# Performance work log

Measured on AMD Instinct MI355X. Metric: run time of the kernel, lower is better.

The kernel has to match this reference:

```python
import jax, jax.numpy as jnp
import numpy as np
from jax.scipy.linalg import solve_triangular, cho_solve

N, NT, O, L1, L2 = 8192, 512, 9, 3, 3
LOG2PI = float(np.log(2.0 * np.pi))


def setup_inputs() -> dict:
    key = jax.random.key(0)
    ks = jax.random.split(key, 10)
    return {
        "y": jax.random.normal(ks[0], (N, NT, O), jnp.float32),
        "b1_r1": 0.5 * jax.random.normal(ks[1], (L1,), jnp.float32),
        "lambda_r1_free": jax.random.normal(ks[2], (6,), jnp.float32),
        "q_r1_diag": jax.random.uniform(ks[3], (L1,), jnp.float32),
        "b1_r2": 0.3 * jax.random.normal(ks[4], (L2, L2), jnp.float32),
        "lambda_r2_free": jax.random.normal(ks[5], (O - 1,), jnp.float32),
        "q_r2_diag": jax.random.uniform(ks[6], (L2,), jnp.float32),
        "r_diag": jax.random.uniform(ks[7], (O,), jnp.float32),
        "gamma1": jnp.array([4.0], jnp.float32),
        "gamma2": jax.random.normal(ks[8], (L1,), jnp.float32),
        "gamma3": jnp.array([4.0], jnp.float32),
        "gamma4": jax.random.normal(ks[9], (L2,), jnp.float32),
    }


def _rskf_nll(y, b1_r1, lambda_r1_free, q_r1_diag, b1_r2, lambda_r2_free,
              q_r2_diag, r_diag, gamma1, gamma2, gamma3, gamma4):
    Nn, Nt, Oo = y.shape
    dt = y.dtype
    # Regime-1 structural matrices (3-factor CFA measurement model)
    B1 = jnp.diag(b1_r1)
    Lam1 = jnp.zeros((Oo, L1), dt)
    Lam1 = Lam1.at[0, 0].set(1.0).at[3, 1].set(1.0).at[6, 2].set(1.0)
    Lam1 = Lam1.at[1, 0].set(lambda_r1_free[0]).at[2, 0].set(lambda_r1_free[1])
    Lam1 = Lam1.at[4, 1].set(lambda_r1_free[2]).at[5, 1].set(lambda_r1_free[3])
    Lam1 = Lam1.at[7, 2].set(lambda_r1_free[4]).at[8, 2].set(lambda_r1_free[5])
    Q1 = jnp.diag(jnp.abs(q_r1_diag) + 1e-4)
    # Regime-2: full transition matrix, 1-factor loading column
    B2 = b1_r2
    Lam2 = jnp.zeros((Oo, L2), dt).at[0, 0].set(1.0).at[1:, 0].set(lambda_r2_free)
    Q2 = jnp.diag(jnp.abs(q_r2_diag) + 1e-4)
    R = jnp.diag(jnp.abs(r_diag) + 1e-4)
    eyeO = jnp.eye(Oo, dtype=dt)

    def regime_step(eta, P, B, Lam, Q, y_t):
        # eta:(N,L) P:(N,L,L) y_t:(N,O)
        L = B.shape[0]
        eta_p = eta @ B.T
        P_p = jnp.einsum('ij,njk,lk->nil', B, P, B) + Q
        mu = eta_p @ Lam.T
        v = y_t - mu
        F = jnp.einsum('ij,njk,lk->nil', Lam, P_p, Lam) + R    # (N,O,O)
        chol = jnp.linalg.cholesky(F)
        z = solve_triangular(chol, v[..., None], lower=True)[..., 0]
        logdet = 2.0 * jnp.sum(jnp.log(jnp.diagonal(chol, axis1=-2, axis2=-1)), axis=-1)
        loglik = -0.5 * (Oo * LOG2PI + logdet + jnp.sum(z * z, axis=-1))
        # F is SPD (R has positive diagonal), so pinv == inverse via Cholesky
        Finv = cho_solve((chol, True), jnp.broadcast_to(eyeO, F.shape))
        K = P_p @ Lam.T @ Finv                                  # (N,L,O)
        eta_f = eta_p + jnp.einsum('nlo,no->nl', K, v)
        ImKL = jnp.eye(L, dtype=dt) - K @ Lam
        P_f = ImKL @ P_p @ jnp.swapaxes(ImKL, -1, -2) + K @ R @ jnp.swapaxes(K, -1, -2)
        return eta_f, P_f, loglik

    def step(carry, y_t):
        eta1, P1, eta2, P2, m_prob, ll = carry
        p11 = jax.nn.sigmoid(gamma1 + eta1 @ gamma2)            # (N,)
        p22 = jax.nn.sigmoid(gamma3 + eta2 @ gamma4)
        T = jnp.stack([jnp.stack([p11, 1.0 - p11], -1),
                       jnp.stack([1.0 - p22, p22], -1)], axis=1)  # (N,2,2)
        m_pred = jnp.einsum('nij,ni->nj', T, m_prob)
        eta1f, P1f, ll1 = regime_step(eta1, P1, B1, Lam1, Q1, y_t)
        eta2f, P2f, ll2 = regime_step(eta2, P2, B2, Lam2, Q2, y_t)
        log_joint = jnp.stack([ll1, ll2], -1) + jnp.log(m_pred + 1e-9)
        log_marg = jax.scipy.special.logsumexp(log_joint, axis=-1)
        m_new = jnp.exp(log_joint - log_marg[:, None])
        return (eta1f, P1f, eta2f, P2f, m_new, ll + log_marg.sum()), None

    eta1_0 = jnp.zeros((Nn, L1), dt)
    P1_0 = jnp.broadcast_to(jnp.eye(L1, dtype=dt) * 1000.0, (Nn, L1, L1))
    eta2_0 = jnp.zeros((Nn, L2), dt)
    P2_0 = jnp.broadcast_to(jnp.eye(L2, dtype=dt) * 1000.0, (Nn, L2, L2))
    m0 = jnp.broadcast_to(jnp.array([0.99, 0.01], dt), (Nn, 2))  # informative prior
    carry0 = (eta1_0, P1_0, eta2_0, P2_0, m0, jnp.zeros((), dt))
    carry, _ = jax.lax.scan(jax.checkpoint(step), carry0, jnp.transpose(y, (1, 0, 2)))
    return -carry[5]


def reference(y, b1_r1, lambda_r1_free, q_r1_diag, b1_r2, lambda_r2_free,
              q_r2_diag, r_diag, gamma1, gamma2, gamma3, gamma4):
    return _rskf_nll(y, b1_r1, lambda_r1_free, q_r1_diag, b1_r2, lambda_r2_free,
                     q_r2_diag, r_diag, gamma1, gamma2, gamma3, gamma4)
```

## Files before the change

### kernel.cpp

```cpp
#include <hip/hip_runtime.h>
#include <math.h>

#define NSUBJ 8192
#define NTT   512
#define OBS   9
#define LOG2PI 1.8378770664093453f

#define CHUNKS   16
#define REALSTEP 32
#define WARMSTEP 32
#define SERIAL_P 48
#define LDS_ENT  68

__global__ void zero_out_kernel(float* out) { out[0] = 0.0f; }

__device__ __forceinline__ float fast_rcp(float x) { return __builtin_amdgcn_rcpf(x); }

__device__ __forceinline__ float swap1(float x) {
    int r = __builtin_amdgcn_update_dpp(0, __float_as_int(x), 0xB1, 0xF, 0xF, true);
    return __int_as_float(r);
}

__global__ __launch_bounds__(64, 1) void precomp_kernel(
    const float* __restrict__ b1_r1, const float* __restrict__ lam1f,
    const float* __restrict__ q1d,   const float* __restrict__ b2_in,
    const float* __restrict__ lam2f, const float* __restrict__ q2d,
    const float* __restrict__ r_in,  float* __restrict__ tab)
{
    const int lane = threadIdx.x;
    const bool is2 = (lane & 1) != 0;

    float Rinv[9];
    float logdetR = 0.0f;
    #pragma unroll
    for (int i = 0; i < 9; ++i) {
        float r = fabsf(r_in[i]) + 1e-4f;
        Rinv[i] = fast_rcp(r);
        logdetR += __logf(r);
    }
    const float C0 = 9.0f * LOG2PI + logdetR;

    float Bm[9];
    {
        float a0 = b1_r1[0], a1 = b1_r1[1], a2 = b1_r1[2];
        Bm[0] = is2 ? b2_in[0] : a0;   Bm[1] = is2 ? b2_in[1] : 0.0f;
        Bm[2] = is2 ? b2_in[2] : 0.0f; Bm[3] = is2 ? b2_in[3] : 0.0f;
        Bm[4] = is2 ? b2_in[4] : a1;   Bm[5] = is2 ? b2_in[5] : 0.0f;
        Bm[6] = is2 ? b2_in[6] : 0.0f; Bm[7] = is2 ? b2_in[7] : 0.0f;
        Bm[8] = is2 ? b2_in[8] : a2;
    }
    float lam[9];
    lam[0] = 1.0f;
    lam[1] = is2 ? lam2f[0] : lam1f[0];
    lam[2] = is2 ? lam2f[1] : lam1f[1];
    lam[3] = is2 ? lam2f[2] : 1.0f;
    lam[4] = is2 ? lam2f[3] : lam1f[2];
    lam[5] = is2 ? lam2f[4] : lam1f[3];
    lam[6] = is2 ? lam2f[5] : 1.0f;
    lam[7] = is2 ? lam2f[6] : lam1f[4];
    lam[8] = is2 ? lam2f[7] : lam1f[5];

    float dA = lam[0]*lam[0]*Rinv[0] + lam[1]*lam[1]*Rinv[1] + lam[2]*lam[2]*Rinv[2];
    float dB = lam[3]*lam[3]*Rinv[3] + lam[4]*lam[4]*Rinv[4] + lam[5]*lam[5]*Rinv[5];
    float dC = lam[6]*lam[6]*Rinv[6] + lam[7]*lam[7]*Rinv[7] + lam[8]*lam[8]*Rinv[8];
    float Dd0 = is2 ? (dA + dB + dC) : dA;
    float Dd1 = is2 ? 0.0f : dB;
    float Dd2 = is2 ? 0.0f : dC;

    float Q0 = fabsf(is2 ? q2d[0] : q1d[0]) + 1e-4f;
    float Q1 = fabsf(is2 ? q2d[1] : q1d[1]) + 1e-4f;
    float Q2 = fabsf(is2 ? q2d[2] : q1d[2]) + 1e-4f;

    float P0 = 1000.0f, P1s = 0.0f, P2s = 0.0f, P3 = 1000.0f, P4 = 0.0f, P5 = 1000.0f;
    float Sv0, Sv1, Sv2, Sv3, Sv4, Sv5, logc;

    #pragma unroll 1
    for (int t = 0; t < SERIAL_P; ++t) {
        float M00 = Bm[0]*P0  + Bm[1]*P1s + Bm[2]*P2s;
        float M01 = Bm[0]*P1s + Bm[1]*P3  + Bm[2]*P4;
        float M02 = Bm[0]*P2s + Bm[1]*P4  + Bm[2]*P5;
        float M10 = Bm[3]*P0  + Bm[4]*P1s + Bm[5]*P2s;
        float M11 = Bm[3]*P1s + Bm[4]*P3  + Bm[5]*P4;
        float M12 = Bm[3]*P2s + Bm[4]*P4  + Bm[5]*P5;
        float M20 = Bm[6]*P0  + Bm[7]*P1s + Bm[8]*P2s;
        float M21 = Bm[6]*P1s + Bm[7]*P3  + Bm[8]*P4;
        float M22 = Bm[6]*P2s + Bm[7]*P4  + Bm[8]*P5;

        float pp00 = M00*Bm[0] + M01*Bm[1] + M02*Bm[2] + Q0;
        float pp01 = M00*Bm[3] + M01*Bm[4] + M02*Bm[5];
        float pp02 = M00*Bm[6] + M01*Bm[7] + M02*Bm[8];
        float pp11 = M10*Bm[3] + M11*Bm[4] + M12*Bm[5] + Q1;
        float pp12 = M10*Bm[6] + M11*Bm[7] + M12*Bm[8];
        float pp22 = M20*Bm[6] + M21*Bm[7] + M22*Bm[8] + Q2;

        float c00 = pp11*pp22 - pp12*pp12;
        float c01 = pp02*pp12 - pp01*pp22;
        float c02 = pp01*pp12 - pp02*pp11;
        float c11 = pp00*pp22 - pp02*pp02;
        float c12 = pp01*pp02 - pp00*pp12;
        float c22 = pp00*pp11 - pp01*pp01;
        float detP = pp00*c00 + pp01*c01 + pp02*c02;
        float idet = fast_rcp(detP);

        float s00 = c00*idet + Dd0;
        float s01 = c01*idet;
        float s02 = c02*idet;
        float s11 = c11*idet + Dd1;
        float s12 = c12*idet;
        float s22 = c22*idet + Dd2;

        float E00 = s11*s22 - s12*s12;
        float E01 = s02*s12 - s01*s22;
        float E02 = s01*s12 - s02*s11;
        float E11 = s00*s22 - s02*s02;
        float E12 = s01*s02 - s00*s12;
        float E22 = s00*s11 - s01*s01;
        float detS = s00*E00 + s01*E01 + s02*E02;
        float idetS = fast_rcp(detS);

        Sv0 = E00*idetS; Sv1 = E01*idetS; Sv2 = E02*idetS;
        Sv3 = E11*idetS; Sv4 = E12*idetS; Sv5 = E22*idetS;
        logc = -0.5f * (C0 + __logf(detP * detS));

        if (lane < 2) {
            float4* tv = (float4*)tab + (size_t)(t * 2 + lane) * 2;
            tv[0] = make_float4(Sv0, Sv1, Sv2, Sv3);
            tv[1] = make_float4(Sv4, Sv5, logc, 0.0f);
        }
        P0 = Sv0; P1s = Sv1; P2s = Sv2; P3 = Sv3; P4 = Sv4; P5 = Sv5;
    }

    const int par = lane & 1;
    for (int t = SERIAL_P + (lane >> 1); t < NTT; t += 32) {
        float4* tv = (float4*)tab + (size_t)(t * 2 + par) * 2;
        tv[0] = make_float4(Sv0, Sv1, Sv2, Sv3);
        tv[1] = make_float4(Sv4, Sv5, logc, 0.0f);
    }
}

__global__ __launch_bounds__(64, 4) void rskf_main(
    const float* __restrict__ y,
    const float* __restrict__ b1_r1, const float* __restrict__ lam1f,
    const float* __restrict__ b2_in, const float* __restrict__ lam2f,
    const float* __restrict__ r_in,
    const float* __restrict__ g1p, const float* __restrict__ g2p,
    const float* __restrict__ g3p, const float* __restrict__ g4p,
    const float* __restrict__ tab_g, float* __restrict__ out)
{
    const int chunk = blockIdx.x & (CHUNKS - 1);
    const int sgrp  = blockIdx.x / CHUNKS;
    const int subj  = sgrp * 32 + (threadIdx.x >> 1);
    const int par   = threadIdx.x & 1;
    const bool is2  = par != 0;

    const int slice0 = (chunk == 0) ? 0 : chunk * REALSTEP - WARMSTEP;
    const int nsteps = (chunk == 0) ? REALSTEP : (WARMSTEP + REALSTEP);
    const int warmN  = nsteps - REALSTEP;

    __shared__ float tab[LDS_ENT * 2 * 8];
    {
        int navail = NTT - slice0;
        int nload4 = (navail < LDS_ENT ? navail : LDS_ENT) * 4;
        const float4* src = (const float4*)tab_g + (size_t)slice0 * 4;
        float4* dst = (float4*)tab;
        #pragma unroll 1
        for (int i = threadIdx.x; i < nload4; i += 64) dst[i] = src[i];
    }
    __syncthreads();

    float Rinv[9];
    #pragma unroll
    for (int i = 0; i < 9; ++i) Rinv[i] = fast_rcp(fabsf(r_in[i]) + 1e-4f);

    float Bm[9];
    {
        float a0 = b1_r1[0], a1 = b1_r1[1], a2 = b1_r1[2];
        Bm[0] = is2 ? b2_in[0] : a0;   Bm[1] = is2 ? b2_in[1] : 0.0f;
        Bm[2] = is2 ? b2_in[2] : 0.0f; Bm[3] = is2 ? b2_in[3] : 0.0f;
        Bm[4] = is2 ? b2_in[4] : a1;   Bm[5] = is2 ? b2_in[5] : 0.0f;
        Bm[6] = is2 ? b2_in[6] : 0.0f; Bm[7] = is2 ? b2_in[7] : 0.0f;
        Bm[8] = is2 ? b2_in[8] : a2;
    }
    float lam[9];
    lam[0] = 1.0f;
    lam[1] = is2 ? lam2f[0] : lam1f[0];
    lam[2] = is2 ? lam2f[1] : lam1f[1];
    lam[3] = is2 ? lam2f[2] : 1.0f;
    lam[4] = is2 ? lam2f[3] : lam1f[2];
    lam[5] = is2 ? lam2f[4] : lam1f[3];
    lam[6] = is2 ? lam2f[5] : 1.0f;
    lam[7] = is2 ? lam2f[6] : lam1f[4];
    lam[8] = is2 ? lam2f[7] : lam1f[5];

    const float gs  = is2 ? g3p[0] : g1p[0];
    const float gv0 = is2 ? g4p[0] : g2p[0];
    const float gv1 = is2 ? g4p[1] : g2p[1];
    const float gv2 = is2 ? g4p[2] : g2p[2];

    float e0 = 0.0f, e1 = 0.0f, e2 = 0.0f;
    float mA = (chunk == 0) ? (is2 ? 0.01f : 0.99f) : 0.5f;
    float mB = 1.0f - mA;
    float llacc = 0.0f;

    const float* ybase = y + (size_t)subj * (NTT * OBS) + (size_t)slice0 * OBS;
    const float* ymax = ybase + (size_t)(nsteps - 2) * OBS;

    float ya[9], yb[9];
    #pragma unroll
    for (int j = 0; j < 9; ++j) { ya[j] = ybase[j]; yb[j] = ybase[9 + j]; }

    const float4* tvp = (const float4*)tab + par * 2;
    float4 taA0 = tvp[0], taA1 = tvp[1];
    float4 taB0 = tvp[4], taB1 = tvp[5];
    const float4* tp = tvp + 8;

    auto step = [&](float (&buf)[9], const float* ldy,
                    float4& ta0, float4& ta1, const float4* tnx, bool real) {
        float S00 = ta0.x, S01 = ta0.y, S02 = ta0.z, S11 = ta0.w;
        float S12 = ta1.x, S22 = ta1.y, logc = ta1.z;
        ta0 = tnx[0];
        ta1 = tnx[1];

        float d   = gs + e0*gv0 + e1*gv1 + e2*gv2;
        float sig = fast_rcp(1.0f + __expf(-d));
        float oth = swap1(sig);
        float mp  = sig * mA + (1.0f - oth) * mB;
        float lmp = __logf(mp + 1e-9f);

        float ep0 = Bm[0]*e0 + Bm[1]*e1 + Bm[2]*e2;
        float ep1 = Bm[3]*e0 + Bm[4]*e1 + Bm[5]*e2;
        float ep2 = Bm[6]*e0 + Bm[7]*e1 + Bm[8]*e2;
        float es1 = is2 ? ep0 : ep1;
        float es2 = is2 ? ep0 : ep2;

        float v0 = buf[0] - lam[0]*ep0;
        float v1 = buf[1] - lam[1]*ep0;
        float v2 = buf[2] - lam[2]*ep0;
        float v3 = buf[3] - lam[3]*es1;
        float v4 = buf[4] - lam[4]*es1;
        float v5 = buf[5] - lam[5]*es1;
        float v6 = buf[6] - lam[6]*es2;
        float v7 = buf[7] - lam[7]*es2;
        float v8 = buf[8] - lam[8]*es2;

        {
            const float* lp = (ldy < ymax) ? ldy : ymax;
            float4 t0, t1;
            __builtin_memcpy(&t0, lp, 16);
            __builtin_memcpy(&t1, lp + 4, 16);
            buf[0] = t0.x; buf[1] = t0.y; buf[2] = t0.z; buf[3] = t0.w;
            buf[4] = t1.x; buf[5] = t1.y; buf[6] = t1.z; buf[7] = t1.w;
            buf[8] = lp[8];
        }

        float vr0 = v0*Rinv[0], vr1 = v1*Rinv[1], vr2 = v2*Rinv[2];
        float vr3 = v3*Rinv[3], vr4 = v4*Rinv[4], vr5 = v5*Rinv[5];
        float vr6 = v6*Rinv[6], vr7 = v7*Rinv[7], vr8 = v8*Rinv[8];
        float vRv = v0*vr0 + v1*vr1 + v2*vr2 + v3*vr3 + v4*vr4
                  + v5*vr5 + v6*vr6 + v7*vr7 + v8*vr8;

        float pA = lam[0]*vr0 + lam[1]*vr1 + lam[2]*vr2;
        float pB = lam[3]*vr3 + lam[4]*vr4 + lam[5]*vr5;
        float pC = lam[6]*vr6 + lam[7]*vr7 + lam[8]*vr8;
        float t0v = is2 ? (pA + pB + pC) : pA;
        float t1v = is2 ? 0.0f : pB;
        float t2v = is2 ? 0.0f : pC;

        float x0 = S00*t0v + S01*t1v + S02*t2v;
        float x1 = S01*t0v + S11*t1v + S12*t2v;
        float x2 = S02*t0v + S12*t1v + S22*t2v;
        float quad = t0v*x0 + t1v*x1 + t2v*x2;

        float llo = logc - 0.5f*vRv + 0.5f*quad;

        e0 = ep0 + x0; e1 = ep1 + x1; e2 = ep2 + x2;

        float lj  = llo + lmp;
        float ljo = swap1(lj);
        float u   = ljo - lj;
        float et  = __expf(-fabsf(u));
        float r   = fast_rcp(1.0f + et);
        if (real) llacc += fmaxf(lj, ljo) + __logf(1.0f + et);
        mA = (u <= 0.0f) ? r : et * r;
        mB = 1.0f - mA;
    };

    const float* pl = ybase + 18;
    int i = 0;
    #pragma unroll 1
    for (; i < warmN; i += 2) {
        step(ya, pl,     taA0, taA1, tp,     false);
        step(yb, pl + 9, taB0, taB1, tp + 4, false);
        pl += 18; tp += 8;
    }
    #pragma unroll 1
    for (; i < nsteps; i += 2) {
        step(ya, pl,     taA0, taA1, tp,     true);
        step(yb, pl + 9, taB0, taB1, tp + 4, true);
        pl += 18; tp += 8;
    }

    float v = llacc;
    v += __shfl_down(v, 32);
    v += __shfl_down(v, 16);
    v += __shfl_down(v, 8);
    v += __shfl_down(v, 4);
    v += __shfl_down(v, 2);
    v += __shfl_down(v, 1);
    if (threadIdx.x == 0) atomicAdd(out, -0.5f * v);
}

extern "C" void kernel_launch(void* const* d_in, const int* in_sizes, int n_in,
                              void* d_out, int out_size, void* d_ws, size_t ws_size,
                              hipStream_t stream) {
    const float* y      = (const float*)d_in[0];
    const float* b1_r1  = (const float*)d_in[1];
    const float* lam1f  = (const float*)d_in[2];
    const float* q1d    = (const float*)d_in[3];
    const float* b2     = (const float*)d_in[4];
    const float* lam2f  = (const float*)d_in[5];
    const float* q2d    = (const float*)d_in[6];
    const float* r_in   = (const float*)d_in[7];
    const float* g1     = (const float*)d_in[8];
    const float* g2     = (const float*)d_in[9];
    const float* g3     = (const float*)d_in[10];
    const float* g4     = (const float*)d_in[11];
    float* out = (float*)d_out;
    float* tab = (float*)d_ws;

    hipLaunchKernelGGL(zero_out_kernel, dim3(1), dim3(1), 0, stream, out);
    hipLaunchKernelGGL(precomp_kernel, dim3(1), dim3(64), 0, stream,
                       b1_r1, lam1f, q1d, b2, lam2f, q2d, r_in, tab);
    hipLaunchKernelGGL(rskf_main, dim3((NSUBJ / 32) * CHUNKS), dim3(64), 0, stream,
                       y, b1_r1, lam1f, b2, lam2f, r_in, g1, g2, g3, g4, tab, out);
}
```

Measured before the change: 328.8 us.

## Load y as coalesced float4 pairs shared via DPP, longer chunks, fold zero-init

The lane pair of each subject now loads four timesteps of y (36 floats) as nine float4s per lane, alternating by parity, and uses DPP broadcasts to give both lanes all eight timesteps per loop body. This replaces per-step scalar and misaligned loads. Time chunks double to 64 real plus 64 warm-up steps, halving the number of chunks, and blocks are reordered so chunk is the high index. Launch bounds drop to 2 waves, and the zeroing of out moves into the precompute kernel to remove one launch. Tradeoffs: more registers (72 broadcast floats per iteration), fewer blocks, and more warm-up work per chunk.

```diff
diff --git a/kernel.cpp b/kernel.cpp
--- a/kernel.cpp
+++ b/kernel.cpp
@@ -6,28 +6,40 @@
 #define OBS   9
 #define LOG2PI 1.8378770664093453f
 
-#define CHUNKS   16
-#define REALSTEP 32
-#define WARMSTEP 32
+#define CHUNKS   8
+#define REALSTEP 64
+#define WARMSTEP 64
 #define SERIAL_P 48
-#define LDS_ENT  68
-
-__global__ void zero_out_kernel(float* out) { out[0] = 0.0f; }
+#define LDS_ENT  132
 
 __device__ __forceinline__ float fast_rcp(float x) { return __builtin_amdgcn_rcpf(x); }
 
 __device__ __forceinline__ float swap1(float x) {
     int r = __builtin_amdgcn_update_dpp(0, __float_as_int(x), 0xB1, 0xF, 0xF, true);
     return __int_as_float(r);
+}
+__device__ __forceinline__ float bcast_even(float x) {
+    int r = __builtin_amdgcn_update_dpp(0, __float_as_int(x), 0xA0, 0xF, 0xF, true);
+    return __int_as_float(r);
+}
+__device__ __forceinline__ float bcast_odd(float x) {
+    int r = __builtin_amdgcn_update_dpp(0, __float_as_int(x), 0xF5, 0xF, 0xF, true);
+    return __int_as_float(r);
+}
+
+__device__ __forceinline__ float f4elem(const float4& v, int j) {
+    return j == 0 ? v.x : j == 1 ? v.y : j == 2 ? v.z : v.w;
 }
 
 __global__ __launch_bounds__(64, 1) void precomp_kernel(
     const float* __restrict__ b1_r1, const float* __restrict__ lam1f,
     const float* __restrict__ q1d,   const float* __restrict__ b2_in,
     const float* __restrict__ lam2f, const float* __restrict__ q2d,
-    const float* __restrict__ r_in,  float* __restrict__ tab)
+    const float* __restrict__ r_in,  float* __restrict__ tab,
+    float* __restrict__ out)
 {
     const int lane = threadIdx.x;
+    if (lane == 0) out[0] = 0.0f;
     const bool is2 = (lane & 1) != 0;
 
     float Rinv[9];
@@ -138,7 +150,7 @@
     }
 }
 
-__global__ __launch_bounds__(64, 4) void rskf_main(
+__global__ __launch_bounds__(64, 2) void rskf_main(
     const float* __restrict__ y,
     const float* __restrict__ b1_r1, const float* __restrict__ lam1f,
     const float* __restrict__ b2_in, const float* __restrict__ lam2f,
@@ -147,15 +159,17 @@
     const float* __restrict__ g3p, const float* __restrict__ g4p,
     const float* __restrict__ tab_g, float* __restrict__ out)
 {
-    const int chunk = blockIdx.x & (CHUNKS - 1);
-    const int sgrp  = blockIdx.x / CHUNKS;
+    const int sgrp  = blockIdx.x & 255;
+    const int chunk = blockIdx.x >> 8;
     const int subj  = sgrp * 32 + (threadIdx.x >> 1);
     const int par   = threadIdx.x & 1;
     const bool is2  = par != 0;
 
     const int slice0 = (chunk == 0) ? 0 : chunk * REALSTEP - WARMSTEP;
     const int nsteps = (chunk == 0) ? REALSTEP : (WARMSTEP + REALSTEP);
-    const int warmN  = nsteps - REALSTEP;
+    const int nbody  = nsteps >> 3;
+    const int warmB  = (nsteps - REALSTEP) >> 3;
+    const int gmax   = (nsteps >> 2) - 1;
 
     __shared__ float tab[LDS_ENT * 2 * 8];
     {
@@ -202,20 +216,21 @@
     float mB = 1.0f - mA;
     float llacc = 0.0f;
 
-    const float* ybase = y + (size_t)subj * (NTT * OBS) + (size_t)slice0 * OBS;
-    const float* ymax = ybase + (size_t)(nsteps - 2) * OBS;
-
-    float ya[9], yb[9];
-    #pragma unroll
-    for (int j = 0; j < 9; ++j) { ya[j] = ybase[j]; yb[j] = ybase[9 + j]; }
+    const float* ysl = y + (size_t)subj * (NTT * OBS) + (size_t)slice0 * OBS;
+
+    float4 raw4[9];
+    {
+        const float4* gp = (const float4*)(ysl + (size_t)par * 36);
+        #pragma unroll
+        for (int i = 0; i < 9; ++i) raw4[i] = gp[i];
+    }
 
     const float4* tvp = (const float4*)tab + par * 2;
     float4 taA0 = tvp[0], taA1 = tvp[1];
     float4 taB0 = tvp[4], taB1 = tvp[5];
-    const float4* tp = tvp + 8;
-
-    auto step = [&](float (&buf)[9], const float* ldy,
-                    float4& ta0, float4& ta1, const float4* tnx, bool real) {
+
+    auto step = [&](const float* yv, float4& ta0, float4& ta1,
+                    const float4* tnx, bool real) {
         float S00 = ta0.x, S01 = ta0.y, S02 = ta0.z, S11 = ta0.w;
         float S12 = ta1.x, S22 = ta1.y, logc = ta1.z;
         ta0 = tnx[0];
@@ -233,25 +248,15 @@
         float es1 = is2 ? ep0 : ep1;
         float es2 = is2 ? ep0 : ep2;
 
-        float v0 = buf[0] - lam[0]*ep0;
-        float v1 = buf[1] - lam[1]*ep0;
-        float v2 = buf[2] - lam[2]*ep0;
-        float v3 = buf[3] - lam[3]*es1;
-        float v4 = buf[4] - lam[4]*es1;
-        float v5 = buf[5] - lam[5]*es1;
-        float v6 = buf[6] - lam[6]*es2;
-        float v7 = buf[7] - lam[7]*es2;
-        float v8 = buf[8] - lam[8]*es2;
-
-        {
-            const float* lp = (ldy < ymax) ? ldy : ymax;
-            float4 t0, t1;
-            __builtin_memcpy(&t0, lp, 16);
-            __builtin_memcpy(&t1, lp + 4, 16);
-            buf[0] = t0.x; buf[1] = t0.y; buf[2] = t0.z; buf[3] = t0.w;
-            buf[4] = t1.x; buf[5] = t1.y; buf[6] = t1.z; buf[7] = t1.w;
-            buf[8] = lp[8];
-        }
+        float v0 = yv[0] - lam[0]*ep0;
+        float v1 = yv[1] - lam[1]*ep0;
+        float v2 = yv[2] - lam[2]*ep0;
+        float v3 = yv[3] - lam[3]*es1;
+        float v4 = yv[4] - lam[4]*es1;
+        float v5 = yv[5] - lam[5]*es1;
+        float v6 = yv[6] - lam[6]*es2;
+        float v7 = yv[7] - lam[7]*es2;
+        float v8 = yv[8] - lam[8]*es2;
 
         float vr0 = v0*Rinv[0], vr1 = v1*Rinv[1], vr2 = v2*Rinv[2];
         float vr3 = v3*Rinv[3], vr4 = v4*Rinv[4], vr5 = v5*Rinv[5];
@@ -280,24 +285,38 @@
         float u   = ljo - lj;
         float et  = __expf(-fabsf(u));
         float r   = fast_rcp(1.0f + et);
-        if (real) llacc += fmaxf(lj, ljo) + __logf(1.0f + et);
+        float lm  = fmaxf(lj, ljo) + __logf(1.0f + et);
+        llacc += real ? lm : 0.0f;
         mA = (u <= 0.0f) ? r : et * r;
         mB = 1.0f - mA;
     };
 
-    const float* pl = ybase + 18;
-    int i = 0;
     #pragma unroll 1
-    for (; i < warmN; i += 2) {
-        step(ya, pl,     taA0, taA1, tp,     false);
-        step(yb, pl + 9, taB0, taB1, tp + 4, false);
-        pl += 18; tp += 8;
-    }
-    #pragma unroll 1
-    for (; i < nsteps; i += 2) {
-        step(ya, pl,     taA0, taA1, tp,     true);
-        step(yb, pl + 9, taB0, taB1, tp + 4, true);
-        pl += 18; tp += 8;
+    for (int b = 0; b < nbody; ++b) {
+        float bcA[36], bcB[36];
+        #pragma unroll
+        for (int j = 0; j < 36; ++j) {
+            float rj = f4elem(raw4[j >> 2], j & 3);
+            bcA[j] = bcast_even(rj);
+            bcB[j] = bcast_odd(rj);
+        }
+        {
+            int ofs = 2 * b + 2 + par;
+            ofs = ofs > gmax ? gmax : ofs;
+            const float4* gp = (const float4*)(ysl + (size_t)ofs * 36);
+            #pragma unroll
+            for (int i = 0; i < 9; ++i) raw4[i] = gp[i];
+        }
+        const bool real = b >= warmB;
+        const float4* tb = tvp + (size_t)(8 * b + 2) * 4;
+        step(&bcA[0],  taA0, taA1, tb,      real);
+        step(&bcA[9],  taB0, taB1, tb + 4,  real);
+        step(&bcA[18], taA0, taA1, tb + 8,  real);
+        step(&bcA[27], taB0, taB1, tb + 12, real);
+        step(&bcB[0],  taA0, taA1, tb + 16, real);
+        step(&bcB[9],  taB0, taB1, tb + 20, real);
+        step(&bcB[18], taA0, taA1, tb + 24, real);
+        step(&bcB[27], taB0, taB1, tb + 28, real);
     }
 
     float v = llacc;
@@ -328,9 +347,8 @@
     float* out = (float*)d_out;
     float* tab = (float*)d_ws;
 
-    hipLaunchKernelGGL(zero_out_kernel, dim3(1), dim3(1), 0, stream, out);
     hipLaunchKernelGGL(precomp_kernel, dim3(1), dim3(64), 0, stream,
-                       b1_r1, lam1f, q1d, b2, lam2f, q2d, r_in, tab);
-    hipLaunchKernelGGL(rskf_main, dim3((NSUBJ / 32) * CHUNKS), dim3(64), 0, stream,
+                       b1_r1, lam1f, q1d, b2, lam2f, q2d, r_in, tab, out);
+    hipLaunchKernelGGL(rskf_main, dim3(256 * CHUNKS), dim3(64), 0, stream,
                        y, b1_r1, lam1f, b2, lam2f, r_in, g1, g2, g3, g4, tab, out);
 }
```

After: 292.8 us. 11.0% less time.
